# Kernel tuning notes

Hardware: AMD Instinct MI355X
Metric: run time of the kernel (lower is better)

Reference implementation:

```python
import jax, jax.numpy as jnp
import numpy as np
import math

N_NODES = 25000
N_EDGES = 400000
FEAT = 128
N_RBF = 20
CUTOFF = 5.0
EPS = 1e-15


def setup_inputs() -> dict:
    key = jax.random.key(0)
    ks = jax.random.split(key, 10)
    s_j = jax.random.normal(ks[0], (N_NODES, FEAT), dtype=jnp.float32)
    v_j = jax.random.normal(ks[1], (N_NODES, FEAT, 3), dtype=jnp.float32)
    r_ij = jax.random.normal(ks[2], (N_EDGES, 3), dtype=jnp.float32)
    nbrs = jax.random.randint(ks[3], (N_EDGES, 2), 0, N_NODES, dtype=jnp.int64)
    # InvariantDense: Linear(F,F) -> swish -> Linear(F,3F)
    sc1 = 1.0 / math.sqrt(FEAT)
    W1 = jax.random.uniform(ks[4], (FEAT, FEAT), jnp.float32, -sc1, sc1)
    b1 = jnp.zeros((FEAT,), jnp.float32)
    W2 = jax.random.uniform(ks[5], (FEAT, 3 * FEAT), jnp.float32, -sc1, sc1)
    b2 = jnp.zeros((3 * FEAT,), jnp.float32)
    # DistanceEmbed dense: Linear(n_rbf, 3F)
    scd = 1.0 / math.sqrt(N_RBF)
    Wd = jax.random.uniform(ks[6], (N_RBF, 3 * FEAT), jnp.float32, -scd, scd)
    bd = jnp.zeros((3 * FEAT,), jnp.float32)
    return {"s_j": s_j, "v_j": v_j, "r_ij": r_ij, "nbrs": nbrs,
            "W1": W1, "b1": b1, "W2": W2, "b2": b2, "Wd": Wd, "bd": bd}


def _swish(x):
    return x * jax.nn.sigmoid(x)


def reference(s_j, v_j, r_ij, nbrs, W1, b1, W2, b2, Wd, bd):
    # preprocess_r
    dist = jnp.sqrt(jnp.sum(r_ij * r_ij + EPS, axis=-1))        # [E]
    unit = r_ij / dist[:, None]                                  # [E, 3]

    src = nbrs[:, 1]
    dst = nbrs[:, 0]

    # invariant dense on gathered scalar features
    s_nb = s_j[src]                                              # [E, F]
    phi = _swish(s_nb @ W1 + b1) @ W2 + b2                       # [E, 3F]

    # radial basis: sin(n*pi*d/cutoff)/d, n = 1..n_rbf
    n = jnp.arange(1, N_RBF + 1, dtype=jnp.float32)
    rbf = jnp.sin(n * jnp.pi / CUTOFF * dist[:, None]) / dist[:, None]  # [E, n_rbf]
    w_s = rbf @ Wd + bd                                          # [E, 3F]

    inv = (phi * w_s).reshape(-1, FEAT, 3)                       # [E, F, 3]
    split0 = inv[:, :, 0:1]                                      # [E, F, 1]
    split1 = inv[:, :, 1]                                        # [E, F]
    split2 = inv[:, :, 2:3]                                      # [E, F, 1]

    delta_v_ij = split2 * unit[:, None, :] + split0 * v_j[src]   # [E, F, 3]
    delta_s_ij = split1                                          # [E, F]

    delta_s_i = jax.ops.segment_sum(delta_s_ij, dst, num_segments=s_j.shape[0])
    delta_v_i = jax.ops.segment_sum(delta_v_ij, dst, num_segments=s_j.shape[0])
    return (delta_s_i, delta_v_i)
```

## Files before the change

kernel.cpp:

```cpp
#include <hip/hip_runtime.h>

namespace {

constexpr int FEAT   = 128;
constexpr int NRBF   = 20;
constexpr int EPB    = 32;
constexpr int NNODES = 25000;
constexpr int NEDGES = 400000;
constexpr int NBLK   = NEDGES / EPB;
constexpr int NPBLK  = (NNODES + 31) / 32;
constexpr int NSCAN  = (NNODES + 255) / 256;
constexpr float PI_F = 3.14159265358979323846f;

using f32x4 = __attribute__((ext_vector_type(4))) float;
using s16x8 = __attribute__((ext_vector_type(8))) short;
using s16x4 = __attribute__((ext_vector_type(4))) short;

constexpr int PW1_ELEMS = 8  * 4 * 64 * 8;
constexpr int PW2_ELEMS = 24 * 4 * 64 * 8;
constexpr int PWD_ELEMS = 24 * 1 * 64 * 8;
constexpr int PW1_OFF = 0;
constexpr int PW2_OFF = PW1_ELEMS;
constexpr int PWD_OFF = PW1_ELEMS + PW2_ELEMS;
constexpr int PT_TOTAL = PW1_ELEMS + PW2_ELEMS + PWD_ELEMS;

__device__ inline unsigned short f2bf(float f) {
    unsigned u = __builtin_bit_cast(unsigned, f);
    u += 0x7fffu + ((u >> 16) & 1u);
    return (unsigned short)(u >> 16);
}
__device__ inline float bf2f(unsigned short h) {
    unsigned u = ((unsigned)h) << 16;
    return __builtin_bit_cast(float, u);
}

__global__ __launch_bounds__(256) void prep_kernel(
    const float* __restrict__ W1, const float* __restrict__ W2,
    const float* __restrict__ Wd, short* __restrict__ pw)
{
    const int idx = blockIdx.x * 256 + threadIdx.x;
    if (idx >= PT_TOTAL) return;
    float val;
    if (idx < PW2_OFF) {
        const int t = idx;
        const int r = t & 7, lane = (t >> 3) & 63, ks = (t >> 9) & 3, nt = t >> 11;
        const int k = ks*32 + (lane>>4)*8 + r, n = nt*16 + (lane & 15);
        val = W1[k*128 + n];
    } else if (idx < PWD_OFF) {
        const int t = idx - PW2_OFF;
        const int r = t & 7, lane = (t >> 3) & 63, ks = (t >> 9) & 3, nt = t >> 11;
        const int k = ks*32 + (lane>>4)*8 + r, n = nt*16 + (lane & 15);
        const int orig = 3*(n & 127) + (n >> 7);
        val = W2[k*384 + orig];
    } else {
        const int t = idx - PWD_OFF;
        const int r = t & 7, lane = (t >> 3) & 63, nt = t >> 9;
        const int k = (lane>>4)*8 + r, n = nt*16 + (lane & 15);
        const int orig = 3*(n & 127) + (n >> 7);
        val = (k < NRBF) ? Wd[k*384 + orig] : 0.f;
    }
    pw[idx] = (short)f2bf(val);
}

__global__ __launch_bounds__(256) void nodephi_kernel(
    const float* __restrict__ s_j, const float* __restrict__ b1,
    const float* __restrict__ b2, const short* __restrict__ pw,
    unsigned short* __restrict__ phiT)
{
    __shared__ short sT[8192];
    constexpr int OFF_H = 4096;
    const int tid = threadIdx.x;
    const int w   = tid >> 6;
    const int l   = tid & 63;
    const int mr  = l & 15;
    const int g   = l >> 4;
    const int n0  = blockIdx.x * 32;

    #pragma unroll
    for (int p = 0; p < 4; ++p) {
        const int v  = tid + p*256;
        const int e  = v >> 5;
        const int c4 = (v & 31) * 4;
        const int node = n0 + e;
        float4 f = {0.f, 0.f, 0.f, 0.f};
        if (node < NNODES)
            f = reinterpret_cast<const float4*>(s_j + (size_t)node*FEAT)[v & 31];
        s16x4 h;
        h.x = (short)f2bf(f.x); h.y = (short)f2bf(f.y);
        h.z = (short)f2bf(f.z); h.w = (short)f2bf(f.w);
        *reinterpret_cast<s16x4*>(&sT[e*128 + (c4 ^ ((e & 7) << 3))]) = h;
    }
    __syncthreads();

    {
        s16x8 aS[2][4];
        #pragma unroll
        for (int mt = 0; mt < 2; ++mt) {
            const int m = mt*16 + mr;
            const int xr = (m & 7) << 3;
            #pragma unroll
            for (int ks = 0; ks < 4; ++ks)
                aS[mt][ks] = *reinterpret_cast<const s16x8*>(&sT[m*128 + ((ks*32 + g*8) ^ xr)]);
        }
        const s16x8* pW1 = reinterpret_cast<const s16x8*>(pw + PW1_OFF);
        #pragma unroll
        for (int i = 0; i < 2; ++i) {
            const int nt = w*2 + i;
            const int n  = nt*16 + mr;
            const float b1n = b1[n];
            f32x4 acc[2] = {f32x4{0,0,0,0}, f32x4{0,0,0,0}};
            #pragma unroll
            for (int ks = 0; ks < 4; ++ks) {
                const s16x8 b = pW1[(nt*4 + ks)*64 + l];
                acc[0] = __builtin_amdgcn_mfma_f32_16x16x32_bf16(aS[0][ks], b, acc[0], 0, 0, 0);
                acc[1] = __builtin_amdgcn_mfma_f32_16x16x32_bf16(aS[1][ks], b, acc[1], 0, 0, 0);
            }
            #pragma unroll
            for (int mt = 0; mt < 2; ++mt)
                #pragma unroll
                for (int r = 0; r < 4; ++r) {
                    const int m = mt*16 + g*4 + r;
                    const float x = acc[mt][r] + b1n;
                    const float hsw = x / (1.0f + __expf(-x));
                    sT[OFF_H + m*128 + (n ^ ((m & 7) << 3))] = (short)f2bf(hsw);
                }
        }
    }
    __syncthreads();

    {
        s16x8 aH[2][4];
        #pragma unroll
        for (int mt = 0; mt < 2; ++mt) {
            const int m = mt*16 + mr;
            const int xr = (m & 7) << 3;
            #pragma unroll
            for (int ks = 0; ks < 4; ++ks)
                aH[mt][ks] = *reinterpret_cast<const s16x8*>(&sT[OFF_H + m*128 + ((ks*32 + g*8) ^ xr)]);
        }
        const s16x8* pW2 = reinterpret_cast<const s16x8*>(pw + PW2_OFF);
        #pragma unroll
        for (int i = 0; i < 6; ++i) {
            const int nt = w*6 + i;
            const int n  = nt*16 + mr;
            const int c  = n >> 7;
            const int f2 = n & 127;
            const float b2n = b2[3*f2 + c];
            f32x4 acc[2] = {f32x4{0,0,0,0}, f32x4{0,0,0,0}};
            #pragma unroll
            for (int ks = 0; ks < 4; ++ks) {
                const s16x8 b = pW2[(nt*4 + ks)*64 + l];
                acc[0] = __builtin_amdgcn_mfma_f32_16x16x32_bf16(aH[0][ks], b, acc[0], 0, 0, 0);
                acc[1] = __builtin_amdgcn_mfma_f32_16x16x32_bf16(aH[1][ks], b, acc[1], 0, 0, 0);
            }
            #pragma unroll
            for (int mt = 0; mt < 2; ++mt)
                #pragma unroll
                for (int r = 0; r < 4; ++r) {
                    const int m = mt*16 + g*4 + r;
                    const int node = n0 + m;
                    if (node < NNODES)
                        phiT[(size_t)c*NNODES*FEAT + (size_t)node*FEAT + f2] =
                            f2bf(acc[mt][r] + b2n);
                }
        }
    }
}

__global__ __launch_bounds__(256) void hist_kernel(
    const int* __restrict__ nbrs, int* __restrict__ hist)
{
    const int e = blockIdx.x * 256 + threadIdx.x;
    if (e >= NEDGES) return;
    const int2 nb = reinterpret_cast<const int2*>(nbrs)[e];
    atomicAdd(&hist[nb.x], 1);
}

__global__ __launch_bounds__(256) void scanA_kernel(
    const int* __restrict__ hist, int* __restrict__ cursor, int* __restrict__ bsum)
{
    __shared__ int sh[256];
    const int t = threadIdx.x, idx = blockIdx.x*256 + t;
    const int v = (idx < NNODES) ? hist[idx] : 0;
    sh[t] = v; __syncthreads();
    int acc = v;
    for (int off = 1; off < 256; off <<= 1) {
        const int add = (t >= off) ? sh[t-off] : 0;
        __syncthreads();
        acc += add; sh[t] = acc;
        __syncthreads();
    }
    if (idx < NNODES) cursor[idx] = acc - v;
    if (t == 255) bsum[blockIdx.x] = acc;
}

__global__ __launch_bounds__(128) void scanB_kernel(
    const int* __restrict__ bsum, int* __restrict__ boffs)
{
    __shared__ int sh[128];
    const int t = threadIdx.x;
    const int v = (t < NSCAN) ? bsum[t] : 0;
    sh[t] = v; __syncthreads();
    int acc = v;
    for (int off = 1; off < 128; off <<= 1) {
        const int add = (t >= off) ? sh[t-off] : 0;
        __syncthreads();
        acc += add; sh[t] = acc;
        __syncthreads();
    }
    if (t < NSCAN) boffs[t] = acc - v;
}

__global__ __launch_bounds__(256) void scanC_kernel(
    int* __restrict__ cursor, const int* __restrict__ boffs)
{
    const int idx = blockIdx.x*256 + threadIdx.x;
    if (idx < NNODES) cursor[idx] += boffs[blockIdx.x];
}

__global__ __launch_bounds__(256) void scatter_kernel(
    const int* __restrict__ nbrs, const float* __restrict__ r_ij,
    int* __restrict__ cursor, int2* __restrict__ recDS, float4* __restrict__ recR)
{
    const int e = blockIdx.x * 256 + threadIdx.x;
    if (e >= NEDGES) return;
    const int2 nb = reinterpret_cast<const int2*>(nbrs)[e];
    const int pos = atomicAdd(&cursor[nb.x], 1);
    recDS[pos] = nb;
    recR[pos] = make_float4(r_ij[3*e+0], r_ij[3*e+1], r_ij[3*e+2], 0.f);
}

__global__ __launch_bounds__(256) void msg_kernel(
    const float* __restrict__ v_j, const int2* __restrict__ recDS,
    const float4* __restrict__ recR, const float* __restrict__ bd,
    const short* __restrict__ pw, const unsigned short* __restrict__ phiT,
    float* __restrict__ ds_out, float* __restrict__ dv_out)
{
    __shared__ short sP[14336];
    __shared__ float sU[EPB][3];
    __shared__ int   sSrc[EPB], sDst[EPB];
    constexpr int OFF_R = 12288;

    const int tid = threadIdx.x;
    const int w   = tid >> 6;
    const int l   = tid & 63;
    const int mr  = l & 15;
    const int g   = l >> 4;
    const int e0  = blockIdx.x * EPB;

    {
        const int ep  = tid >> 3;
        const int sub = tid & 7;
        const int2  nb = recDS[e0 + ep];
        const float4 r = recR[e0 + ep];
        const float d     = sqrtf(r.x*r.x + r.y*r.y + r.z*r.z + 3e-15f);
        const float inv_d = 1.0f / d;
        if (sub == 0) {
            sDst[ep] = nb.x; sSrc[ep] = nb.y;
            sU[ep][0] = r.x*inv_d; sU[ep][1] = r.y*inv_d; sU[ep][2] = r.z*inv_d;
        }
        s16x8 rv;
        #pragma unroll
        for (int kk = 0; kk < 8; ++kk) {
            const int k = sub*8 + kk;
            const float v = (k < NRBF) ? __sinf((float)(k+1)*(PI_F/5.0f)*d)*inv_d : 0.f;
            rv[kk] = (short)f2bf(v);
        }
        *reinterpret_cast<s16x8*>(&sP[OFF_R + ep*64 + ((sub*8) ^ ((ep & 7) << 3))]) = rv;
    }

    #pragma unroll
    for (int pl = 0; pl < 3; ++pl) {
        #pragma unroll
        for (int p = 0; p < 2; ++p) {
            const int v  = tid + p*256;
            const int e  = v >> 4;
            const int ch = (v & 15) * 8;
            const int src = recDS[e0 + e].y;
            const s16x8 val = *reinterpret_cast<const s16x8*>(
                phiT + (size_t)pl*NNODES*FEAT + (size_t)src*FEAT + ch);
            *reinterpret_cast<s16x8*>(&sP[pl*4096 + e*128 + (ch ^ ((e & 7) << 3))]) = val;
        }
    }
    __syncthreads();

    {
        s16x8 aR[2];
        #pragma unroll
        for (int mt = 0; mt < 2; ++mt) {
            const int m = mt*16 + mr;
            aR[mt] = *reinterpret_cast<const s16x8*>(&sP[OFF_R + m*64 + ((g*8) ^ ((m & 7) << 3))]);
        }
        const s16x8* pWd = reinterpret_cast<const s16x8*>(pw + PWD_OFF);
        #pragma unroll
        for (int i = 0; i < 6; ++i) {
            const int nt = w*6 + i;
            const int n  = nt*16 + mr;
            const int c  = n >> 7;
            const int f2 = n & 127;
            const float bdn = bd[3*f2 + c];
            const s16x8 bw = pWd[nt*64 + l];
            f32x4 accw[2] = {f32x4{0,0,0,0}, f32x4{0,0,0,0}};
            accw[0] = __builtin_amdgcn_mfma_f32_16x16x32_bf16(aR[0], bw, accw[0], 0, 0, 0);
            accw[1] = __builtin_amdgcn_mfma_f32_16x16x32_bf16(aR[1], bw, accw[1], 0, 0, 0);
            #pragma unroll
            for (int mt = 0; mt < 2; ++mt)
                #pragma unroll
                for (int r = 0; r < 4; ++r) {
                    const int m = mt*16 + g*4 + r;
                    const int addr = c*4096 + m*128 + (f2 ^ ((m & 7) << 3));
                    const float phi = bf2f((unsigned short)sP[addr]);
                    sP[addr] = (short)f2bf(phi * (accw[mt][r] + bdn));
                }
        }
    }
    __syncthreads();

    {
        const int half = tid >> 7;
        const int f    = tid & 127;
        const int eb   = half * 16;
        float accS = 0.f, a0 = 0.f, a1 = 0.f, a2 = 0.f;
        int cur = sDst[eb];
        #pragma unroll 4
        for (int e = eb; e < eb + 16; ++e) {
            const int d = sDst[e];
            if (d != cur) {
                atomicAdd(ds_out + (size_t)cur*FEAT + f, accS);
                float* dvp = dv_out + (size_t)cur*(3*FEAT) + 3*f;
                atomicAdd(dvp + 0, a0);
                atomicAdd(dvp + 1, a1);
                atomicAdd(dvp + 2, a2);
                accS = a0 = a1 = a2 = 0.f;
                cur = d;
            }
            const int fx = f ^ ((e & 7) << 3);
            const float i0 = bf2f((unsigned short)sP[        e*128 + fx]);
            const float i1 = bf2f((unsigned short)sP[4096 + e*128 + fx]);
            const float i2 = bf2f((unsigned short)sP[8192 + e*128 + fx]);
            const int src = sSrc[e];
            const float* vj = v_j + (size_t)src*(3*FEAT) + 3*f;
            const float u0 = sU[e][0], u1 = sU[e][1], u2 = sU[e][2];
            accS += i1;
            a0 += i2*u0 + i0*vj[0];
            a1 += i2*u1 + i0*vj[1];
            a2 += i2*u2 + i0*vj[2];
        }
        atomicAdd(ds_out + (size_t)cur*FEAT + f, accS);
        float* dvp = dv_out + (size_t)cur*(3*FEAT) + 3*f;
        atomicAdd(dvp + 0, a0);
        atomicAdd(dvp + 1, a1);
        atomicAdd(dvp + 2, a2);
    }
}

}

extern "C" void kernel_launch(void* const* d_in, const int* in_sizes, int n_in,
                              void* d_out, int out_size, void* d_ws, size_t ws_size,
                              hipStream_t stream)
{
    const float* s_j  = (const float*)d_in[0];
    const float* v_j  = (const float*)d_in[1];
    const float* r_ij = (const float*)d_in[2];
    const int*   nbrs = (const int*)d_in[3];
    const float* W1   = (const float*)d_in[4];
    const float* b1   = (const float*)d_in[5];
    const float* W2   = (const float*)d_in[6];
    const float* b2   = (const float*)d_in[7];
    const float* Wd   = (const float*)d_in[8];
    const float* bd   = (const float*)d_in[9];

    float* ds_out = (float*)d_out;
    float* dv_out = ds_out + (size_t)NNODES * FEAT;

    char* base = (char*)d_ws;
    short* pw            = (short*)base;
    int*   hist          = (int*)(base + 160*1024);
    int*   cursor        = (int*)(base + 272*1024);
    int*   bsum          = (int*)(base + 376*1024);
    int*   boffs         = (int*)(base + 380*1024);
    int2*  recDS         = (int2*)(base + 512*1024);
    float4* recR         = (float4*)(base + 4ull*1024*1024);
    unsigned short* phiT = (unsigned short*)(base + 16ull*1024*1024);

    hipMemsetAsync(d_out, 0, (size_t)out_size * sizeof(float), stream);
    hipMemsetAsync(hist, 0, NNODES * sizeof(int), stream);

    prep_kernel<<<(PT_TOTAL + 255)/256, 256, 0, stream>>>(W1, W2, Wd, pw);
    nodephi_kernel<<<NPBLK, 256, 0, stream>>>(s_j, b1, b2, pw, phiT);
    hist_kernel<<<(NEDGES + 255)/256, 256, 0, stream>>>(nbrs, hist);
    scanA_kernel<<<NSCAN, 256, 0, stream>>>(hist, cursor, bsum);
    scanB_kernel<<<1, 128, 0, stream>>>(bsum, boffs);
    scanC_kernel<<<NSCAN, 256, 0, stream>>>(cursor, boffs);
    scatter_kernel<<<(NEDGES + 255)/256, 256, 0, stream>>>(nbrs, r_ij, cursor, recDS, recR);

    msg_kernel<<<NBLK, 256, 0, stream>>>(
        v_j, recDS, recR, bd, pw, phiT, ds_out, dv_out);
}
```

Measured before the change: 408.6 us.

## Fuse prep/hist and nodephi/scan kernels, batch v_j gathers in message loop

```diff
diff --git a/kernel.cpp b/kernel.cpp
--- a/kernel.cpp
+++ b/kernel.cpp
@@ -9,7 +9,6 @@
 constexpr int NEDGES = 400000;
 constexpr int NBLK   = NEDGES / EPB;
 constexpr int NPBLK  = (NNODES + 31) / 32;
-constexpr int NSCAN  = (NNODES + 255) / 256;
 constexpr float PI_F = 3.14159265358979323846f;
 
 using f32x4 = __attribute__((ext_vector_type(4))) float;
@@ -23,6 +22,8 @@
 constexpr int PW2_OFF = PW1_ELEMS;
 constexpr int PWD_OFF = PW1_ELEMS + PW2_ELEMS;
 constexpr int PT_TOTAL = PW1_ELEMS + PW2_ELEMS + PWD_ELEMS;
+constexpr int PREP_BLKS = (PT_TOTAL + 255) / 256;
+constexpr int HIST_BLKS = (NEDGES + 255) / 256;
 
 __device__ inline unsigned short f2bf(float f) {
     unsigned u = __builtin_bit_cast(unsigned, f);
@@ -34,39 +35,75 @@
     return __builtin_bit_cast(float, u);
 }
 
-__global__ __launch_bounds__(256) void prep_kernel(
+__global__ __launch_bounds__(256) void k1_prep_hist(
     const float* __restrict__ W1, const float* __restrict__ W2,
-    const float* __restrict__ Wd, short* __restrict__ pw)
-{
-    const int idx = blockIdx.x * 256 + threadIdx.x;
-    if (idx >= PT_TOTAL) return;
-    float val;
-    if (idx < PW2_OFF) {
-        const int t = idx;
-        const int r = t & 7, lane = (t >> 3) & 63, ks = (t >> 9) & 3, nt = t >> 11;
-        const int k = ks*32 + (lane>>4)*8 + r, n = nt*16 + (lane & 15);
-        val = W1[k*128 + n];
-    } else if (idx < PWD_OFF) {
-        const int t = idx - PW2_OFF;
-        const int r = t & 7, lane = (t >> 3) & 63, ks = (t >> 9) & 3, nt = t >> 11;
-        const int k = ks*32 + (lane>>4)*8 + r, n = nt*16 + (lane & 15);
-        const int orig = 3*(n & 127) + (n >> 7);
-        val = W2[k*384 + orig];
+    const float* __restrict__ Wd, short* __restrict__ pw,
+    const int* __restrict__ nbrs, int* __restrict__ hist)
+{
+    if (blockIdx.x < PREP_BLKS) {
+        const int idx = blockIdx.x * 256 + threadIdx.x;
+        if (idx >= PT_TOTAL) return;
+        float val;
+        if (idx < PW2_OFF) {
+            const int t = idx;
+            const int r = t & 7, lane = (t >> 3) & 63, ks = (t >> 9) & 3, nt = t >> 11;
+            const int k = ks*32 + (lane>>4)*8 + r, n = nt*16 + (lane & 15);
+            val = W1[k*128 + n];
+        } else if (idx < PWD_OFF) {
+            const int t = idx - PW2_OFF;
+            const int r = t & 7, lane = (t >> 3) & 63, ks = (t >> 9) & 3, nt = t >> 11;
+            const int k = ks*32 + (lane>>4)*8 + r, n = nt*16 + (lane & 15);
+            const int orig = 3*(n & 127) + (n >> 7);
+            val = W2[k*384 + orig];
+        } else {
+            const int t = idx - PWD_OFF;
+            const int r = t & 7, lane = (t >> 3) & 63, nt = t >> 9;
+            const int k = (lane>>4)*8 + r, n = nt*16 + (lane & 15);
+            const int orig = 3*(n & 127) + (n >> 7);
+            val = (k < NRBF) ? Wd[k*384 + orig] : 0.f;
+        }
+        pw[idx] = (short)f2bf(val);
     } else {
-        const int t = idx - PWD_OFF;
-        const int r = t & 7, lane = (t >> 3) & 63, nt = t >> 9;
-        const int k = (lane>>4)*8 + r, n = nt*16 + (lane & 15);
-        const int orig = 3*(n & 127) + (n >> 7);
-        val = (k < NRBF) ? Wd[k*384 + orig] : 0.f;
-    }
-    pw[idx] = (short)f2bf(val);
-}
-
-__global__ __launch_bounds__(256) void nodephi_kernel(
+        const int e = (blockIdx.x - PREP_BLKS) * 256 + threadIdx.x;
+        if (e >= NEDGES) return;
+        const int2 nb = reinterpret_cast<const int2*>(nbrs)[e];
+        atomicAdd(&hist[nb.x], 1);
+    }
+}
+
+__global__ __launch_bounds__(256) void k2_nodephi_scan(
     const float* __restrict__ s_j, const float* __restrict__ b1,
     const float* __restrict__ b2, const short* __restrict__ pw,
-    unsigned short* __restrict__ phiT)
-{
+    unsigned short* __restrict__ phiT,
+    const int* __restrict__ hist, int* __restrict__ cursor)
+{
+    if (blockIdx.x == NPBLK) {
+        __shared__ int part[256];
+        const int t = threadIdx.x;
+        constexpr int CH = (NNODES + 255) / 256;
+        const int base = t * CH;
+        int s = 0;
+        for (int i = 0; i < CH; ++i) {
+            const int idx = base + i;
+            if (idx < NNODES) s += hist[idx];
+        }
+        part[t] = s;
+        __syncthreads();
+        for (int off = 1; off < 256; off <<= 1) {
+            int v = part[t];
+            if (t >= off) v += part[t - off];
+            __syncthreads();
+            part[t] = v;
+            __syncthreads();
+        }
+        int run = part[t] - s;
+        for (int i = 0; i < CH; ++i) {
+            const int idx = base + i;
+            if (idx < NNODES) { cursor[idx] = run; run += hist[idx]; }
+        }
+        return;
+    }
+
     __shared__ short sT[8192];
     constexpr int OFF_H = 4096;
     const int tid = threadIdx.x;
@@ -167,57 +204,6 @@
     }
 }
 
-__global__ __launch_bounds__(256) void hist_kernel(
-    const int* __restrict__ nbrs, int* __restrict__ hist)
-{
-    const int e = blockIdx.x * 256 + threadIdx.x;
-    if (e >= NEDGES) return;
-    const int2 nb = reinterpret_cast<const int2*>(nbrs)[e];
-    atomicAdd(&hist[nb.x], 1);
-}
-
-__global__ __launch_bounds__(256) void scanA_kernel(
-    const int* __restrict__ hist, int* __restrict__ cursor, int* __restrict__ bsum)
-{
-    __shared__ int sh[256];
-    const int t = threadIdx.x, idx = blockIdx.x*256 + t;
-    const int v = (idx < NNODES) ? hist[idx] : 0;
-    sh[t] = v; __syncthreads();
-    int acc = v;
-    for (int off = 1; off < 256; off <<= 1) {
-        const int add = (t >= off) ? sh[t-off] : 0;
-        __syncthreads();
-        acc += add; sh[t] = acc;
-        __syncthreads();
-    }
-    if (idx < NNODES) cursor[idx] = acc - v;
-    if (t == 255) bsum[blockIdx.x] = acc;
-}
-
-__global__ __launch_bounds__(128) void scanB_kernel(
-    const int* __restrict__ bsum, int* __restrict__ boffs)
-{
-    __shared__ int sh[128];
-    const int t = threadIdx.x;
-    const int v = (t < NSCAN) ? bsum[t] : 0;
-    sh[t] = v; __syncthreads();
-    int acc = v;
-    for (int off = 1; off < 128; off <<= 1) {
-        const int add = (t >= off) ? sh[t-off] : 0;
-        __syncthreads();
-        acc += add; sh[t] = acc;
-        __syncthreads();
-    }
-    if (t < NSCAN) boffs[t] = acc - v;
-}
-
-__global__ __launch_bounds__(256) void scanC_kernel(
-    int* __restrict__ cursor, const int* __restrict__ boffs)
-{
-    const int idx = blockIdx.x*256 + threadIdx.x;
-    if (idx < NNODES) cursor[idx] += boffs[blockIdx.x];
-}
-
 __global__ __launch_bounds__(256) void scatter_kernel(
     const int* __restrict__ nbrs, const float* __restrict__ r_ij,
     int* __restrict__ cursor, int2* __restrict__ recDS, float4* __restrict__ recR)
@@ -322,29 +308,38 @@
         const int eb   = half * 16;
         float accS = 0.f, a0 = 0.f, a1 = 0.f, a2 = 0.f;
         int cur = sDst[eb];
-        #pragma unroll 4
-        for (int e = eb; e < eb + 16; ++e) {
-            const int d = sDst[e];
-            if (d != cur) {
-                atomicAdd(ds_out + (size_t)cur*FEAT + f, accS);
-                float* dvp = dv_out + (size_t)cur*(3*FEAT) + 3*f;
-                atomicAdd(dvp + 0, a0);
-                atomicAdd(dvp + 1, a1);
-                atomicAdd(dvp + 2, a2);
-                accS = a0 = a1 = a2 = 0.f;
-                cur = d;
+        #pragma unroll
+        for (int chunk = 0; chunk < 2; ++chunk) {
+            float vx[8], vy[8], vz[8];
+            #pragma unroll
+            for (int j = 0; j < 8; ++j) {
+                const int e = eb + chunk*8 + j;
+                const float* vj = v_j + (size_t)sSrc[e]*(3*FEAT) + 3*f;
+                vx[j] = vj[0]; vy[j] = vj[1]; vz[j] = vj[2];
             }
-            const int fx = f ^ ((e & 7) << 3);
-            const float i0 = bf2f((unsigned short)sP[        e*128 + fx]);
-            const float i1 = bf2f((unsigned short)sP[4096 + e*128 + fx]);
-            const float i2 = bf2f((unsigned short)sP[8192 + e*128 + fx]);
-            const int src = sSrc[e];
-            const float* vj = v_j + (size_t)src*(3*FEAT) + 3*f;
-            const float u0 = sU[e][0], u1 = sU[e][1], u2 = sU[e][2];
-            accS += i1;
-            a0 += i2*u0 + i0*vj[0];
-            a1 += i2*u1 + i0*vj[1];
-            a2 += i2*u2 + i0*vj[2];
+            #pragma unroll
+            for (int j = 0; j < 8; ++j) {
+                const int e = eb + chunk*8 + j;
+                const int d = sDst[e];
+                if (d != cur) {
+                    atomicAdd(ds_out + (size_t)cur*FEAT + f, accS);
+                    float* dvp = dv_out + (size_t)cur*(3*FEAT) + 3*f;
+                    atomicAdd(dvp + 0, a0);
+                    atomicAdd(dvp + 1, a1);
+                    atomicAdd(dvp + 2, a2);
+                    accS = a0 = a1 = a2 = 0.f;
+                    cur = d;
+                }
+                const int fx = f ^ ((e & 7) << 3);
+                const float i0 = bf2f((unsigned short)sP[        e*128 + fx]);
+                const float i1 = bf2f((unsigned short)sP[4096 + e*128 + fx]);
+                const float i2 = bf2f((unsigned short)sP[8192 + e*128 + fx]);
+                const float u0 = sU[e][0], u1 = sU[e][1], u2 = sU[e][2];
+                accS += i1;
+                a0 += i2*u0 + i0*vx[j];
+                a1 += i2*u1 + i0*vy[j];
+                a2 += i2*u2 + i0*vz[j];
+            }
         }
         atomicAdd(ds_out + (size_t)cur*FEAT + f, accS);
         float* dvp = dv_out + (size_t)cur*(3*FEAT) + 3*f;
@@ -378,8 +373,6 @@
     short* pw            = (short*)base;
     int*   hist          = (int*)(base + 160*1024);
     int*   cursor        = (int*)(base + 272*1024);
-    int*   bsum          = (int*)(base + 376*1024);
-    int*   boffs         = (int*)(base + 380*1024);
     int2*  recDS         = (int2*)(base + 512*1024);
     float4* recR         = (float4*)(base + 4ull*1024*1024);
     unsigned short* phiT = (unsigned short*)(base + 16ull*1024*1024);
@@ -387,13 +380,12 @@
     hipMemsetAsync(d_out, 0, (size_t)out_size * sizeof(float), stream);
     hipMemsetAsync(hist, 0, NNODES * sizeof(int), stream);
 
-    prep_kernel<<<(PT_TOTAL + 255)/256, 256, 0, stream>>>(W1, W2, Wd, pw);
-    nodephi_kernel<<<NPBLK, 256, 0, stream>>>(s_j, b1, b2, pw, phiT);
-    hist_kernel<<<(NEDGES + 255)/256, 256, 0, stream>>>(nbrs, hist);
-    scanA_kernel<<<NSCAN, 256, 0, stream>>>(hist, cursor, bsum);
-    scanB_kernel<<<1, 128, 0, stream>>>(bsum, boffs);
-    scanC_kernel<<<NSCAN, 256, 0, stream>>>(cursor, boffs);
-    scatter_kernel<<<(NEDGES + 255)/256, 256, 0, stream>>>(nbrs, r_ij, cursor, recDS, recR);
+    k1_prep_hist<<<PREP_BLKS + HIST_BLKS, 256, 0, stream>>>(
+        W1, W2, Wd, pw, nbrs, hist);
+    k2_nodephi_scan<<<NPBLK + 1, 256, 0, stream>>>(
+        s_j, b1, b2, pw, phiT, hist, cursor);
+    scatter_kernel<<<(NEDGES + 255)/256, 256, 0, stream>>>(
+        nbrs, r_ij, cursor, recDS, recR);
 
     msg_kernel<<<NBLK, 256, 0, stream>>>(
         v_j, recDS, recR, bd, pw, phiT, ds_out, dv_out);
```

After: 437.8 us. 1.07x slower.
